# Kernel tuning notes

Hardware: AMD Instinct MI355X
Metric: run time of the kernel (lower is better)

Reference implementation:

```python
import jax, jax.numpy as jnp
import numpy as np

B, H, W, C = 1, 64, 64, 768
HEADS = 12
HD = C // HEADS  # 64


def setup_inputs() -> dict:
    key = jax.random.key(0)
    ks = jax.random.split(key, 11)
    s = 0.02
    return {
        "hidden_states": jax.random.normal(ks[0], (B, H, W, C), jnp.float32),
        "w_q": jax.random.normal(ks[1], (C, C), jnp.float32) * s,
        "b_q": jnp.zeros((C,), jnp.float32),
        "w_k": jax.random.normal(ks[2], (C, C), jnp.float32) * s,
        "b_k": jnp.zeros((C,), jnp.float32),
        "w_v": jax.random.normal(ks[3], (C, C), jnp.float32) * s,
        "b_v": jnp.zeros((C,), jnp.float32),
        "w_o": jax.random.normal(ks[4], (C, C), jnp.float32) * s,
        "b_o": jnp.zeros((C,), jnp.float32),
        "rel_pos_h": jax.random.normal(ks[5], (2 * H - 1, HD), jnp.float32) * s,
        "rel_pos_w": jax.random.normal(ks[6], (2 * W - 1, HD), jnp.float32) * s,
    }


def _get_rel_pos(q_size, k_size, rel_pos):
    # q_size == k_size here, so no interpolation branch; pure gather.
    coords = jnp.arange(q_size)[:, None] - jnp.arange(k_size)[None, :] + (k_size - 1)
    return rel_pos[coords]  # (q_size, k_size, head_dim)


def reference(hidden_states, w_q, b_q, w_k, b_k, w_v, b_v, w_o, b_o, rel_pos_h, rel_pos_w):
    b, h, w, c = hidden_states.shape
    hd = c // HEADS

    def proj(wm, bm):
        y = hidden_states @ wm.T + bm  # (b,h,w,c)
        return y.reshape(b, h * w, HEADS, hd).transpose(0, 2, 1, 3)  # (b,heads,hw,hd)

    q = proj(w_q, b_q)
    k = proj(w_k, b_k)
    v = proj(w_v, b_v)

    # decomposed relative position bias (per head-dim query)
    Rh = _get_rel_pos(h, h, rel_pos_h)  # (h,h,hd)
    Rw = _get_rel_pos(w, w, rel_pos_w)  # (w,w,hd)
    qr = q.reshape(b, HEADS, h, w, hd)
    rel_h = jnp.einsum('bnhwc,hkc->bnhwk', qr, Rh)  # (b,heads,h,w,h)
    rel_w = jnp.einsum('bnhwc,wkc->bnhwk', qr, Rw)  # (b,heads,h,w,w)
    attn_bias = (rel_h[..., :, None] + rel_w[..., None, :]).reshape(b, HEADS, h * w, h * w)

    scale = hd ** -0.5
    scores = jnp.einsum('bnqd,bnkd->bnqk', q, k) * scale + attn_bias
    attn = jax.nn.softmax(scores, axis=-1)
    out = jnp.einsum('bnqk,bnkd->bnqd', attn, v)  # (b,heads,hw,hd)
    out = out.transpose(0, 2, 1, 3).reshape(b, h, w, c)
    return out @ w_o.T + b_o
```

## Files before the change

kernel.cpp:

```cpp
#include <hip/hip_runtime.h>


typedef __attribute__((ext_vector_type(8))) short bf16x8;
typedef __attribute__((ext_vector_type(4))) float f32x4;
typedef __attribute__((ext_vector_type(4))) short s16x4;
typedef __attribute__((ext_vector_type(2))) unsigned int u32x2;

__device__ __forceinline__ float b2f(unsigned short h) {
    union { unsigned int u; float f; } v; v.u = ((unsigned int)h) << 16; return v.f;
}
__device__ __forceinline__ unsigned short f2b(float f) {
    union { float f; unsigned int u; } v; v.f = f;
    unsigned int r = v.u + 0x7FFFu + ((v.u >> 16) & 1u);
    return (unsigned short)(r >> 16);
}
__device__ __forceinline__ void gl_lds16(const void* g, void* l) {
    __builtin_amdgcn_global_load_lds(
        (const __attribute__((address_space(1))) void*)g,
        (__attribute__((address_space(3))) void*)l, 16, 0, 0);
}

__global__ __launch_bounds__(256) void cvt_bf16(
        const float* __restrict__ hs, const float* __restrict__ wq,
        const float* __restrict__ wk, const float* __restrict__ wv,
        const float* __restrict__ wo, const float* __restrict__ rph,
        const float* __restrict__ rpw, unsigned short* __restrict__ dst) {
    const int idx = blockIdx.x * 256 + threadIdx.x;
    if (idx >= 1380320) return;
    const float* src;
    int off;
    if      (idx < 786432)  { src = hs;  off = idx; }
    else if (idx < 933888)  { src = wq;  off = idx - 786432; }
    else if (idx < 1081344) { src = wk;  off = idx - 933888; }
    else if (idx < 1228800) { src = wv;  off = idx - 1081344; }
    else if (idx < 1376256) { src = wo;  off = idx - 1228800; }
    else if (idx < 1378288) { src = rph; off = idx - 1376256; }
    else                    { src = rpw; off = idx - 1378288; }
    const float4 v = ((const float4*)src)[off];
    s16x4 o;
    o[0] = (short)f2b(v.x); o[1] = (short)f2b(v.y);
    o[2] = (short)f2b(v.z); o[3] = (short)f2b(v.w);
    *(s16x4*)(dst + (size_t)idx * 4) = o;
}

__launch_bounds__(256, 3)
__global__ void qkv128(const unsigned short* __restrict__ X,
                       const unsigned short* __restrict__ Wq,
                       const unsigned short* __restrict__ Wk,
                       const unsigned short* __restrict__ Wv,
                       const float* __restrict__ bq,
                       const float* __restrict__ bk,
                       const float* __restrict__ bv,
                       unsigned short* __restrict__ qb,
                       unsigned short* __restrict__ kb,
                       unsigned short* __restrict__ vtb) {
    __shared__ __align__(16) unsigned short sarena[16384];
    const int tid = threadIdx.x, lane = tid & 63, w = tid >> 6;
    const int r = lane & 15, quad = lane >> 4;
    const int nt = blockIdx.x, mt = blockIdx.y, z = blockIdx.z;
    const unsigned short* W  = (z == 0) ? Wq : (z == 1) ? Wk : Wv;
    const float*          Bv = (z == 0) ? bq : (z == 1) ? bk : bv;
    unsigned short*     outp = (z == 0) ? qb : (z == 1) ? kb : vtb;
    const float qsc = (z == 0) ? 0.18033688f : 1.0f;

    const int c0 = w * 64 + lane, c1 = c0 + 256;
    const unsigned short* xs0 = X + (mt * 128 + (c0 & 127)) * 768 + (c0 >> 7) * 8;
    const unsigned short* xs1 = X + (mt * 128 + (c1 & 127)) * 768 + (c1 >> 7) * 8;
    const unsigned short* ws0 = W + (nt * 128 + (c0 & 127)) * 768 + (c0 >> 7) * 8;
    const unsigned short* ws1 = W + (nt * 128 + (c1 & 127)) * 768 + (c1 >> 7) * 8;

    gl_lds16(xs0, &sarena[w * 512]);
    gl_lds16(xs1, &sarena[2048 + w * 512]);
    gl_lds16(ws0, &sarena[4096 + w * 512]);
    gl_lds16(ws1, &sarena[4096 + 2048 + w * 512]);
    __syncthreads();

    const int wr = (w & 1) * 64, wc = (w >> 1) * 64;
    f32x4 acc[4][4] = {};
    int cur = 0;
#pragma unroll 2
    for (int kt = 0; kt < 24; ++kt) {
        if (kt < 23) {
            const int nx = (cur ^ 1) * 8192;
            gl_lds16(xs0 + (kt + 1) * 32, &sarena[nx + w * 512]);
            gl_lds16(xs1 + (kt + 1) * 32, &sarena[nx + 2048 + w * 512]);
            gl_lds16(ws0 + (kt + 1) * 32, &sarena[nx + 4096 + w * 512]);
            gl_lds16(ws1 + (kt + 1) * 32, &sarena[nx + 4096 + 2048 + w * 512]);
        }
        const unsigned short* ab = &sarena[cur * 8192];
        const unsigned short* bb = ab + 4096;
        bf16x8 af[4], bfr[4];
#pragma unroll
        for (int i = 0; i < 4; ++i)
            af[i] = *(const bf16x8*)&ab[(quad * 128 + wr + i * 16 + r) * 8];
#pragma unroll
        for (int j = 0; j < 4; ++j)
            bfr[j] = *(const bf16x8*)&bb[(quad * 128 + wc + j * 16 + r) * 8];
#pragma unroll
        for (int i = 0; i < 4; ++i)
#pragma unroll
            for (int j = 0; j < 4; ++j)
                acc[i][j] = __builtin_amdgcn_mfma_f32_16x16x32_bf16(af[i], bfr[j], acc[i][j], 0, 0, 0);
        __syncthreads();
        cur ^= 1;
    }
    if (z < 2) {
#pragma unroll
        for (int j = 0; j < 4; ++j) {
            const int n = nt * 128 + wc + j * 16 + r;
            const float bias = Bv[n];
            const int nhi = n >> 6, nlo = n & 63;
#pragma unroll
            for (int i = 0; i < 4; ++i) {
#pragma unroll
                for (int reg = 0; reg < 4; ++reg) {
                    const int m = mt * 128 + wr + i * 16 + quad * 4 + reg;
                    outp[(nhi * 4096 + m) * 64 + nlo] = f2b((acc[i][j][reg] + bias) * qsc);
                }
            }
        }
    } else {
#pragma unroll
        for (int pass = 0; pass < 2; ++pass) {
            if ((w >> 1) == pass) {
#pragma unroll
                for (int j = 0; j < 4; ++j) {
                    const int n_l = j * 16 + r;
                    const float bias = Bv[nt * 128 + pass * 64 + n_l];
                    const int sw = (n_l & 7) << 4;
#pragma unroll
                    for (int reg = 0; reg < 4; ++reg) {
                        const int tokb = (wr + (quad * 4 + reg) * 4) ^ sw;
                        u32x2 d2;
                        d2.x = (unsigned int)f2b(acc[0][j][reg] + bias)
                             | ((unsigned int)f2b(acc[1][j][reg] + bias) << 16);
                        d2.y = (unsigned int)f2b(acc[2][j][reg] + bias)
                             | ((unsigned int)f2b(acc[3][j][reg] + bias) << 16);
                        *(u32x2*)&sarena[n_l * 128 + tokb] = d2;
                    }
                }
            }
            __syncthreads();
#pragma unroll
            for (int c = 0; c < 4; ++c) {
                const int u = c * 256 + tid;
                const int n_l = u >> 4, g = u & 15;
                const int phys = n_l * 128 + ((g * 8) ^ ((n_l & 7) << 4));
                bf16x8 val = *(const bf16x8*)&sarena[phys];
                *(bf16x8*)&outp[(size_t)(nt * 128 + pass * 64 + n_l) * 4096
                                + mt * 128 + g * 8] = val;
            }
            __syncthreads();
        }
    }
}

__launch_bounds__(256, 3)
__global__ void out128(const unsigned short* __restrict__ X,
                       const unsigned short* __restrict__ W,
                       const float* __restrict__ Bv,
                       float* __restrict__ out) {
    __shared__ __align__(16) unsigned short sarena[16384];
    const int tid = threadIdx.x, lane = tid & 63, w = tid >> 6;
    const int r = lane & 15, quad = lane >> 4;
    const int nt = blockIdx.x, mt = blockIdx.y;

    const int c0 = w * 64 + lane, c1 = c0 + 256;
    const unsigned short* xs0 = X + (mt * 128 + (c0 & 127)) * 768 + (c0 >> 7) * 8;
    const unsigned short* xs1 = X + (mt * 128 + (c1 & 127)) * 768 + (c1 >> 7) * 8;
    const unsigned short* ws0 = W + (nt * 128 + (c0 & 127)) * 768 + (c0 >> 7) * 8;
    const unsigned short* ws1 = W + (nt * 128 + (c1 & 127)) * 768 + (c1 >> 7) * 8;

    gl_lds16(xs0, &sarena[w * 512]);
    gl_lds16(xs1, &sarena[2048 + w * 512]);
    gl_lds16(ws0, &sarena[4096 + w * 512]);
    gl_lds16(ws1, &sarena[4096 + 2048 + w * 512]);
    __syncthreads();

    const int wr = (w & 1) * 64, wc = (w >> 1) * 64;
    f32x4 acc[4][4] = {};
    int cur = 0;
#pragma unroll 2
    for (int kt = 0; kt < 24; ++kt) {
        if (kt < 23) {
            const int nx = (cur ^ 1) * 8192;
            gl_lds16(xs0 + (kt + 1) * 32, &sarena[nx + w * 512]);
            gl_lds16(xs1 + (kt + 1) * 32, &sarena[nx + 2048 + w * 512]);
            gl_lds16(ws0 + (kt + 1) * 32, &sarena[nx + 4096 + w * 512]);
            gl_lds16(ws1 + (kt + 1) * 32, &sarena[nx + 4096 + 2048 + w * 512]);
        }
        const unsigned short* ab = &sarena[cur * 8192];
        const unsigned short* bb = ab + 4096;
        bf16x8 af[4], bfr[4];
#pragma unroll
        for (int i = 0; i < 4; ++i)
            af[i] = *(const bf16x8*)&ab[(quad * 128 + wr + i * 16 + r) * 8];
#pragma unroll
        for (int j = 0; j < 4; ++j)
            bfr[j] = *(const bf16x8*)&bb[(quad * 128 + wc + j * 16 + r) * 8];
#pragma unroll
        for (int i = 0; i < 4; ++i)
#pragma unroll
            for (int j = 0; j < 4; ++j)
                acc[i][j] = __builtin_amdgcn_mfma_f32_16x16x32_bf16(af[i], bfr[j], acc[i][j], 0, 0, 0);
        __syncthreads();
        cur ^= 1;
    }
#pragma unroll
    for (int j = 0; j < 4; ++j) {
        const int n = nt * 128 + wc + j * 16 + r;
        const float bias = Bv[n];
#pragma unroll
        for (int i = 0; i < 4; ++i) {
#pragma unroll
            for (int reg = 0; reg < 4; ++reg) {
                const int m = mt * 128 + wr + i * 16 + quad * 4 + reg;
                out[m * 768 + n] = acc[i][j][reg] + bias;
            }
        }
    }
}

__launch_bounds__(256, 4)
__global__ void relk(const unsigned short* __restrict__ qbuf,
                     const unsigned short* __restrict__ rph,
                     const unsigned short* __restrict__ rpw,
                     unsigned short* __restrict__ rh,
                     unsigned short* __restrict__ rw) {
    __shared__ __align__(16) unsigned short abuf[8 * 64 * 8];
    __shared__ __align__(16) unsigned short bbuf[8 * 64 * 8];
    const int tid = threadIdx.x;
    const int lane = tid & 63, w = tid >> 6;
    const int r = lane & 15, quad = lane >> 4;
    const int a = blockIdx.x, h = blockIdx.y, mode = blockIdx.z;
    const unsigned short* rp = mode ? rpw : rph;
    const float osc = 8.0f;

#pragma unroll
    for (int gg = 0; gg < 2; ++gg) {
        const int g = w * 2 + gg;
        const int arow = mode ? (h * 4096 + lane * 64 + a) : (h * 4096 + a * 64 + lane);
        gl_lds16(qbuf + arow * 64 + g * 8, &abuf[g * 512]);
        const int bidx = a - lane + 63;
        gl_lds16(rp + bidx * 64 + g * 8, &bbuf[g * 512]);
    }
    __syncthreads();

    f32x4 acc[4] = {};
#pragma unroll
    for (int s = 0; s < 2; ++s) {
        bf16x8 af = *(const bf16x8*)&abuf[((s * 4 + quad) * 64 + w * 16 + r) * 8];
#pragma unroll
        for (int j = 0; j < 4; ++j) {
            bf16x8 bfr = *(const bf16x8*)&bbuf[((s * 4 + quad) * 64 + j * 16 + r) * 8];
            acc[j] = __builtin_amdgcn_mfma_f32_16x16x32_bf16(af, bfr, acc[j], 0, 0, 0);
        }
    }
    unsigned short* out = mode ? rw : rh;
#pragma unroll
    for (int j = 0; j < 4; ++j) {
#pragma unroll
        for (int reg = 0; reg < 4; ++reg) {
            const int m = w * 16 + quad * 4 + reg, n = j * 16 + r;
            const int t = mode ? (h * 4096 + m * 64 + a) : (h * 4096 + a * 64 + m);
            out[t * 64 + n] = f2b(acc[j][reg] * osc);
        }
    }
}

__launch_bounds__(256, 3)
__global__ void attn2(const unsigned short* __restrict__ qbuf,
                      const unsigned short* __restrict__ kbuf,
                      const unsigned short* __restrict__ vtbuf,
                      const unsigned short* __restrict__ rhb,
                      const unsigned short* __restrict__ rwb,
                      float* __restrict__ po, float* __restrict__ lp) {
    __shared__ __align__(16) unsigned short skb[2][4096];
    __shared__ __align__(16) unsigned short svb[2][4096];
    __shared__ __align__(16) unsigned short spb[9216];
    const int tid = threadIdx.x;
    const int lane = tid & 63, w = tid >> 6;
    const int r = lane & 15, quad = lane >> 4;
    const int qt = blockIdx.x, h = blockIdx.y, sp = blockIdx.z;

    {
        const int t0 = sp * 32;
#pragma unroll
        for (int gg = 0; gg < 2; ++gg) {
            const int g = w * 2 + gg;
            gl_lds16(kbuf + (h * 4096 + t0 * 64 + lane) * 64 + g * 8, &skb[0][g * 512]);
            gl_lds16(vtbuf + (h * 64 + lane) * 4096 + t0 * 64 + g * 8, &svb[0][g * 512]);
        }
    }
    const unsigned short* rhp =
        rhb + (size_t)(h * 4096 + qt * 128 + w * 16 + quad * 4) * 64;
    unsigned short rhu[8];
#pragma unroll
    for (int i = 0; i < 8; ++i)
        rhu[i] = rhp[((i >> 2) * 64 + (i & 3)) * 64 + sp * 32];

    bf16x8 qf[2][2];
#pragma unroll
    for (int g = 0; g < 2; ++g) {
        const unsigned short* qrow =
            qbuf + (h * 4096 + qt * 128 + g * 64 + w * 16 + r) * 64;
        qf[g][0] = *(const bf16x8*)(qrow + quad * 8);
        qf[g][1] = *(const bf16x8*)(qrow + 32 + quad * 8);
    }
    float rwL[2][4][4];
#pragma unroll
    for (int g = 0; g < 2; ++g) {
        const unsigned short* rwrow = rwb + (h * 4096 + qt * 128 + g * 64) * 64;
#pragma unroll
        for (int reg = 0; reg < 4; ++reg) {
            const int ql = w * 16 + quad * 4 + reg;
#pragma unroll
            for (int j = 0; j < 4; ++j)
                rwL[g][j][reg] = b2f(rwrow[ql * 64 + j * 16 + r]);
        }
    }
    bf16x8 onesf;
#pragma unroll
    for (int i = 0; i < 8; ++i) onesf[i] = (short)0x3F80;

    f32x4 lacc[2] = {};
    f32x4 oacc[2][4] = {};
    __syncthreads();

    int cur = 0;
#pragma unroll 2
    for (int tl = 0; tl < 32; ++tl) {
        const int t = sp * 32 + tl;
        if (tl < 31) {
#pragma unroll
            for (int gg = 0; gg < 2; ++gg) {
                const int g = w * 2 + gg;
                gl_lds16(kbuf + (h * 4096 + (t + 1) * 64 + lane) * 64 + g * 8,
                         &skb[cur ^ 1][g * 512]);
                gl_lds16(vtbuf + (h * 64 + lane) * 4096 + (t + 1) * 64 + g * 8,
                         &svb[cur ^ 1][g * 512]);
            }
        }
        float rh2f[8];
#pragma unroll
        for (int i = 0; i < 8; ++i) rh2f[i] = b2f(rhu[i]);
        if (tl < 31) {
#pragma unroll
            for (int i = 0; i < 8; ++i)
                rhu[i] = rhp[((i >> 2) * 64 + (i & 3)) * 64 + (t + 1)];
        }
        f32x4 s0[4], s1[4];
#pragma unroll
        for (int j = 0; j < 4; ++j)
#pragma unroll
            for (int reg = 0; reg < 4; ++reg) {
                s0[j][reg] = rh2f[reg]     + rwL[0][j][reg];
                s1[j][reg] = rh2f[4 + reg] + rwL[1][j][reg];
            }
        __builtin_amdgcn_s_setprio(1);
#pragma unroll
        for (int s2 = 0; s2 < 2; ++s2) {
#pragma unroll
            for (int j = 0; j < 4; ++j) {
                bf16x8 kf = *(const bf16x8*)&skb[cur][((s2 * 4 + quad) * 64 + j * 16 + r) * 8];
                s0[j] = __builtin_amdgcn_mfma_f32_16x16x32_bf16(qf[0][s2], kf, s0[j], 0, 0, 0);
                s1[j] = __builtin_amdgcn_mfma_f32_16x16x32_bf16(qf[1][s2], kf, s1[j], 0, 0, 0);
            }
        }
        __builtin_amdgcn_s_setprio(0);
#pragma unroll
        for (int g = 0; g < 2; ++g) {
#pragma unroll
            for (int reg = 0; reg < 4; ++reg) {
                unsigned int u[4];
#pragma unroll
                for (int j = 0; j < 4; ++j) {
                    const float p = __builtin_amdgcn_exp2f(g ? s1[j][reg] : s0[j][reg]);
                    union { float f; unsigned int q; } cv; cv.f = p;
                    u[j] = cv.q;
                }
                u32x2 d;
                d.x = __builtin_amdgcn_perm(u[1], u[0], 0x07060302);
                d.y = __builtin_amdgcn_perm(u[3], u[2], 0x07060302);
                *(u32x2*)&spb[g * 4608 + w * 1152 + (quad * 4 + reg) * 72 + r * 4] = d;
            }
        }
        __builtin_amdgcn_s_setprio(1);
#pragma unroll
        for (int s = 0; s < 2; ++s) {
            bf16x8 pf0 = *(const bf16x8*)&spb[w * 1152 + r * 72 + s * 32 + quad * 8];
            bf16x8 pf1 = *(const bf16x8*)&spb[4608 + w * 1152 + r * 72 + s * 32 + quad * 8];
            lacc[0] = __builtin_amdgcn_mfma_f32_16x16x32_bf16(pf0, onesf, lacc[0], 0, 0, 0);
            lacc[1] = __builtin_amdgcn_mfma_f32_16x16x32_bf16(pf1, onesf, lacc[1], 0, 0, 0);
#pragma unroll
            for (int j = 0; j < 4; ++j) {
                bf16x8 vf = *(const bf16x8*)&svb[cur][((s * 4 + quad) * 64 + j * 16 + r) * 8];
                oacc[0][j] = __builtin_amdgcn_mfma_f32_16x16x32_bf16(pf0, vf, oacc[0][j], 0, 0, 0);
                oacc[1][j] = __builtin_amdgcn_mfma_f32_16x16x32_bf16(pf1, vf, oacc[1][j], 0, 0, 0);
            }
        }
        __builtin_amdgcn_s_setprio(0);

        __syncthreads();
        cur ^= 1;
    }
    const size_t pbase = ((size_t)(sp * 12 + h) * 4096 + qt * 128);
#pragma unroll
    for (int g = 0; g < 2; ++g) {
        const int qrow = g * 64 + w * 16 + quad * 4;
#pragma unroll
        for (int reg = 0; reg < 4; ++reg) {
#pragma unroll
            for (int j = 0; j < 4; ++j)
                po[(pbase + qrow + reg) * 64 + j * 16 + r] = oacc[g][j][reg];
            if (r == 0) lp[pbase + qrow + reg] = lacc[g][reg];
        }
    }
}

__global__ __launch_bounds__(256) void combine(const float* __restrict__ po,
                                               const float* __restrict__ lp,
                                               unsigned short* __restrict__ ab) {
    const unsigned int idx = blockIdx.x * 256 + threadIdx.x;
    const unsigned int tok = idx / 96u;
    const unsigned int part = idx - tok * 96u;
    const int c = part * 8, h = c >> 6, d = c & 63;
    const float* p0 = po + ((size_t)h * 4096 + tok) * 64 + d;
    const float* p1 = po + ((size_t)(12 + h) * 4096 + tok) * 64 + d;
    const float inv = 1.f / (lp[h * 4096 + tok] + lp[(12 + h) * 4096 + tok]);
    const float4 a0 = *(const float4*)p0, b0 = *(const float4*)(p0 + 4);
    const float4 a1 = *(const float4*)p1, b1 = *(const float4*)(p1 + 4);
    s16x4 o0, o1;
    o0[0] = (short)f2b((a0.x + a1.x) * inv); o0[1] = (short)f2b((a0.y + a1.y) * inv);
    o0[2] = (short)f2b((a0.z + a1.z) * inv); o0[3] = (short)f2b((a0.w + a1.w) * inv);
    o1[0] = (short)f2b((b0.x + b1.x) * inv); o1[1] = (short)f2b((b0.y + b1.y) * inv);
    o1[2] = (short)f2b((b0.z + b1.z) * inv); o1[3] = (short)f2b((b0.w + b1.w) * inv);
    unsigned short* dst = ab + (size_t)tok * 768 + c;
    *(s16x4*)dst = o0;
    *(s16x4*)(dst + 4) = o1;
}

extern "C" void kernel_launch(void* const* d_in, const int* in_sizes, int n_in,
                              void* d_out, int out_size, void* d_ws, size_t ws_size,
                              hipStream_t stream) {
    const float* hs  = (const float*)d_in[0];
    const float* wq  = (const float*)d_in[1];
    const float* bq  = (const float*)d_in[2];
    const float* wk  = (const float*)d_in[3];
    const float* bk  = (const float*)d_in[4];
    const float* wv  = (const float*)d_in[5];
    const float* bv  = (const float*)d_in[6];
    const float* wo  = (const float*)d_in[7];
    const float* bo  = (const float*)d_in[8];
    const float* rph = (const float*)d_in[9];
    const float* rpw = (const float*)d_in[10];

    unsigned short* ws = (unsigned short*)d_ws;
    const int HS = 3145728, WN = 589824, RP = 8128;
    const int HB = 12 * 4096 * 64;
    unsigned short* hsb  = ws;
    unsigned short* wqb  = hsb  + HS;
    unsigned short* wkb  = wqb  + WN;
    unsigned short* wvb  = wkb  + WN;
    unsigned short* wob  = wvb  + WN;
    unsigned short* rphb = wob  + WN;
    unsigned short* rpwb = rphb + RP;
    unsigned short* qb   = rpwb + RP;
    unsigned short* kb   = qb   + HB;
    unsigned short* vtb  = kb   + HB;
    unsigned short* rhb  = vtb  + HB;
    unsigned short* rwb  = rhb  + HB;
    unsigned short* ab   = rwb  + HB;
    float* po = (float*)(ab + HB);
    float* lp = po + 2 * 12 * 4096 * 64;

    cvt_bf16<<<dim3((1380320 + 255) / 256), 256, 0, stream>>>(
        hs, wq, wk, wv, wo, rph, rpw, hsb);
    qkv128<<<dim3(6, 32, 3), 256, 0, stream>>>(
        hsb, wqb, wkb, wvb, bq, bk, bv, qb, kb, vtb);
    relk<<<dim3(64, 12, 2), 256, 0, stream>>>(qb, rphb, rpwb, rhb, rwb);
    attn2<<<dim3(32, 12, 2), 256, 0, stream>>>(qb, kb, vtb, rhb, rwb, po, lp);
    combine<<<dim3(1536), 256, 0, stream>>>(po, lp, ab);
    out128<<<dim3(6, 32), 256, 0, stream>>>(ab, wob, bo, (float*)d_out);
}
```

Measured before the change: 241.0 us.

## Prefetch K/V tiles through registers into single LDS buffer

Replaces the double-buffered direct global-to-LDS async loads of K and V tiles with register prefetch: the next tile is loaded into registers during compute, then written to a single LDS buffer after a barrier. This halves LDS use for K/V, which could allow more resident blocks, and uses wider 16-byte-per-lane loads. In exchange it adds a second __syncthreads per iteration, extra VGPR pressure, and explicit LDS store instructions, and it drops the unroll-by-2.

```diff
diff --git a/kernel.cpp b/kernel.cpp
--- a/kernel.cpp
+++ b/kernel.cpp
@@ -5,6 +5,7 @@
 typedef __attribute__((ext_vector_type(4))) float f32x4;
 typedef __attribute__((ext_vector_type(4))) short s16x4;
 typedef __attribute__((ext_vector_type(2))) unsigned int u32x2;
+typedef __attribute__((ext_vector_type(4))) unsigned int u32x4;
 
 __device__ __forceinline__ float b2f(unsigned short h) {
     union { unsigned int u; float f; } v; v.u = ((unsigned int)h) << 16; return v.f;
@@ -275,22 +276,23 @@
                       const unsigned short* __restrict__ rhb,
                       const unsigned short* __restrict__ rwb,
                       float* __restrict__ po, float* __restrict__ lp) {
-    __shared__ __align__(16) unsigned short skb[2][4096];
-    __shared__ __align__(16) unsigned short svb[2][4096];
+    __shared__ __align__(16) unsigned short skb[4096];
+    __shared__ __align__(16) unsigned short svb[4096];
     __shared__ __align__(16) unsigned short spb[9216];
     const int tid = threadIdx.x;
     const int lane = tid & 63, w = tid >> 6;
     const int r = lane & 15, quad = lane >> 4;
     const int qt = blockIdx.x, h = blockIdx.y, sp = blockIdx.z;
 
+    const unsigned short* ksrc = kbuf + (size_t)(h * 4096 + lane) * 64 + w * 16;
+    const unsigned short* vsrc = vtbuf + (size_t)(h * 64 + lane) * 4096 + w * 16;
+    u32x4 kp0, kp1, vp0, vp1;
     {
         const int t0 = sp * 32;
-#pragma unroll
-        for (int gg = 0; gg < 2; ++gg) {
-            const int g = w * 2 + gg;
-            gl_lds16(kbuf + (h * 4096 + t0 * 64 + lane) * 64 + g * 8, &skb[0][g * 512]);
-            gl_lds16(vtbuf + (h * 64 + lane) * 4096 + t0 * 64 + g * 8, &svb[0][g * 512]);
-        }
+        kp0 = *(const u32x4*)(ksrc + (size_t)t0 * 4096);
+        kp1 = *(const u32x4*)(ksrc + (size_t)t0 * 4096 + 8);
+        vp0 = *(const u32x4*)(vsrc + t0 * 64);
+        vp1 = *(const u32x4*)(vsrc + t0 * 64 + 8);
     }
     const unsigned short* rhp =
         rhb + (size_t)(h * 4096 + qt * 128 + w * 16 + quad * 4) * 64;
@@ -325,21 +327,19 @@
 
     f32x4 lacc[2] = {};
     f32x4 oacc[2][4] = {};
+    *(u32x4*)&skb[(w * 128 + lane) * 8]      = kp0;
+    *(u32x4*)&skb[(w * 128 + 64 + lane) * 8] = kp1;
+    *(u32x4*)&svb[(w * 128 + lane) * 8]      = vp0;
+    *(u32x4*)&svb[(w * 128 + 64 + lane) * 8] = vp1;
     __syncthreads();
 
-    int cur = 0;
-#pragma unroll 2
     for (int tl = 0; tl < 32; ++tl) {
         const int t = sp * 32 + tl;
         if (tl < 31) {
-#pragma unroll
-            for (int gg = 0; gg < 2; ++gg) {
-                const int g = w * 2 + gg;
-                gl_lds16(kbuf + (h * 4096 + (t + 1) * 64 + lane) * 64 + g * 8,
-                         &skb[cur ^ 1][g * 512]);
-                gl_lds16(vtbuf + (h * 64 + lane) * 4096 + (t + 1) * 64 + g * 8,
-                         &svb[cur ^ 1][g * 512]);
-            }
+            kp0 = *(const u32x4*)(ksrc + (size_t)(t + 1) * 4096);
+            kp1 = *(const u32x4*)(ksrc + (size_t)(t + 1) * 4096 + 8);
+            vp0 = *(const u32x4*)(vsrc + (t + 1) * 64);
+            vp1 = *(const u32x4*)(vsrc + (t + 1) * 64 + 8);
         }
         float rh2f[8];
 #pragma unroll
@@ -362,7 +362,7 @@
         for (int s2 = 0; s2 < 2; ++s2) {
 #pragma unroll
             for (int j = 0; j < 4; ++j) {
-                bf16x8 kf = *(const bf16x8*)&skb[cur][((s2 * 4 + quad) * 64 + j * 16 + r) * 8];
+                bf16x8 kf = *(const bf16x8*)&skb[((s2 * 4 + quad) * 64 + j * 16 + r) * 8];
                 s0[j] = __builtin_amdgcn_mfma_f32_16x16x32_bf16(qf[0][s2], kf, s0[j], 0, 0, 0);
                 s1[j] = __builtin_amdgcn_mfma_f32_16x16x32_bf16(qf[1][s2], kf, s1[j], 0, 0, 0);
             }
@@ -394,7 +394,7 @@
             lacc[1] = __builtin_amdgcn_mfma_f32_16x16x32_bf16(pf1, onesf, lacc[1], 0, 0, 0);
 #pragma unroll
             for (int j = 0; j < 4; ++j) {
-                bf16x8 vf = *(const bf16x8*)&svb[cur][((s * 4 + quad) * 64 + j * 16 + r) * 8];
+                bf16x8 vf = *(const bf16x8*)&svb[((s * 4 + quad) * 64 + j * 16 + r) * 8];
                 oacc[0][j] = __builtin_amdgcn_mfma_f32_16x16x32_bf16(pf0, vf, oacc[0][j], 0, 0, 0);
                 oacc[1][j] = __builtin_amdgcn_mfma_f32_16x16x32_bf16(pf1, vf, oacc[1][j], 0, 0, 0);
             }
@@ -402,7 +402,13 @@
         __builtin_amdgcn_s_setprio(0);
 
         __syncthreads();
-        cur ^= 1;
+        if (tl < 31) {
+            *(u32x4*)&skb[(w * 128 + lane) * 8]      = kp0;
+            *(u32x4*)&skb[(w * 128 + 64 + lane) * 8] = kp1;
+            *(u32x4*)&svb[(w * 128 + lane) * 8]      = vp0;
+            *(u32x4*)&svb[(w * 128 + 64 + lane) * 8] = vp1;
+        }
+        __syncthreads();
     }
     const size_t pbase = ((size_t)(sp * 12 + h) * 4096 + qt * 128);
 #pragma unroll
```

After: 242.1 us. About the same (+0.5%).

## Load K/V fragments directly to registers and swizzle attention block order

Applied to the files above, without the earlier changes.

The attention kernel stops staging K and V tiles through double-buffered LDS with per-iteration barriers. Each lane now loads its MFMA K/V fragments straight from global memory into registers, prefetching the next K tile during compute. The rel-h bias slice is preloaded into LDS once instead of being fetched per iteration. The grid is flattened and remapped so blocks sharing the same head/K-range are spread across XCDs for L2 locality. The cost is more global/L2 traffic per block, since K/V are no longer shared across waves, plus extra register pressure.

```diff
diff --git a/kernel.cpp b/kernel.cpp
--- a/kernel.cpp
+++ b/kernel.cpp
@@ -275,30 +275,21 @@
                       const unsigned short* __restrict__ rhb,
                       const unsigned short* __restrict__ rwb,
                       float* __restrict__ po, float* __restrict__ lp) {
-    __shared__ __align__(16) unsigned short skb[2][4096];
-    __shared__ __align__(16) unsigned short svb[2][4096];
     __shared__ __align__(16) unsigned short spb[9216];
+    __shared__ __align__(16) unsigned short srh[4096];
     const int tid = threadIdx.x;
     const int lane = tid & 63, w = tid >> 6;
     const int r = lane & 15, quad = lane >> 4;
-    const int qt = blockIdx.x, h = blockIdx.y, sp = blockIdx.z;
-
-    {
-        const int t0 = sp * 32;
-#pragma unroll
-        for (int gg = 0; gg < 2; ++gg) {
-            const int g = w * 2 + gg;
-            gl_lds16(kbuf + (h * 4096 + t0 * 64 + lane) * 64 + g * 8, &skb[0][g * 512]);
-            gl_lds16(vtbuf + (h * 64 + lane) * 4096 + t0 * 64 + g * 8, &svb[0][g * 512]);
-        }
-    }
-    const unsigned short* rhp =
-        rhb + (size_t)(h * 4096 + qt * 128 + w * 16 + quad * 4) * 64;
-    unsigned short rhu[8];
-#pragma unroll
-    for (int i = 0; i < 8; ++i)
-        rhu[i] = rhp[((i >> 2) * 64 + (i & 3)) * 64 + sp * 32];
-
+    const int bid = blockIdx.x;
+    const int g768 = (bid & 7) * 96 + (bid >> 3);
+    const int h = g768 >> 6, sp = (g768 >> 5) & 1, qt = g768 & 31;
+
+#pragma unroll
+    for (int i = 0; i < 2; ++i) {
+        const int ql = (w & 1) * 64 + lane;
+        gl_lds16(rhb + (h * 4096 + qt * 128 + ql) * 64 + (sp * 4 + i * 2 + (w >> 1)) * 8,
+                 &srh[(i * 256 + w * 64) * 8]);
+    }
     bf16x8 qf[2][2];
 #pragma unroll
     for (int g = 0; g < 2; ++g) {
@@ -323,32 +314,29 @@
 #pragma unroll
     for (int i = 0; i < 8; ++i) onesf[i] = (short)0x3F80;
 
+    const unsigned short* klane = kbuf + ((size_t)h * 4096 + r) * 64 + quad * 8;
+    const unsigned short* vlane = vtbuf + ((size_t)h * 64 + r) * 4096 + quad * 8;
+
     f32x4 lacc[2] = {};
     f32x4 oacc[2][4] = {};
     __syncthreads();
 
-    int cur = 0;
-#pragma unroll 2
+    bf16x8 kf[8], vf[8];
+    {
+        const int t0 = sp * 32;
+#pragma unroll
+        for (int i = 0; i < 8; ++i)
+            kf[i] = *(const bf16x8*)(klane + (size_t)t0 * 4096
+                                     + (i & 3) * 1024 + (i >> 2) * 32);
+    }
+
     for (int tl = 0; tl < 32; ++tl) {
         const int t = sp * 32 + tl;
-        if (tl < 31) {
-#pragma unroll
-            for (int gg = 0; gg < 2; ++gg) {
-                const int g = w * 2 + gg;
-                gl_lds16(kbuf + (h * 4096 + (t + 1) * 64 + lane) * 64 + g * 8,
-                         &skb[cur ^ 1][g * 512]);
-                gl_lds16(vtbuf + (h * 64 + lane) * 4096 + (t + 1) * 64 + g * 8,
-                         &svb[cur ^ 1][g * 512]);
-            }
-        }
         float rh2f[8];
 #pragma unroll
-        for (int i = 0; i < 8; ++i) rh2f[i] = b2f(rhu[i]);
-        if (tl < 31) {
-#pragma unroll
-            for (int i = 0; i < 8; ++i)
-                rhu[i] = rhp[((i >> 2) * 64 + (i & 3)) * 64 + (t + 1)];
-        }
+        for (int i = 0; i < 8; ++i)
+            rh2f[i] = b2f(srh[((tl >> 3) * 128 + (i >> 2) * 64 + w * 16
+                               + quad * 4 + (i & 3)) * 8 + (t & 7)]);
         f32x4 s0[4], s1[4];
 #pragma unroll
         for (int j = 0; j < 4; ++j)
@@ -362,12 +350,21 @@
         for (int s2 = 0; s2 < 2; ++s2) {
 #pragma unroll
             for (int j = 0; j < 4; ++j) {
-                bf16x8 kf = *(const bf16x8*)&skb[cur][((s2 * 4 + quad) * 64 + j * 16 + r) * 8];
-                s0[j] = __builtin_amdgcn_mfma_f32_16x16x32_bf16(qf[0][s2], kf, s0[j], 0, 0, 0);
-                s1[j] = __builtin_amdgcn_mfma_f32_16x16x32_bf16(qf[1][s2], kf, s1[j], 0, 0, 0);
+                s0[j] = __builtin_amdgcn_mfma_f32_16x16x32_bf16(qf[0][s2], kf[s2 * 4 + j], s0[j], 0, 0, 0);
+                s1[j] = __builtin_amdgcn_mfma_f32_16x16x32_bf16(qf[1][s2], kf[s2 * 4 + j], s1[j], 0, 0, 0);
             }
         }
         __builtin_amdgcn_s_setprio(0);
+#pragma unroll
+        for (int i = 0; i < 8; ++i)
+            vf[i] = *(const bf16x8*)(vlane + (size_t)(i & 3) * 65536
+                                     + t * 64 + (i >> 2) * 32);
+        if (tl < 31) {
+#pragma unroll
+            for (int i = 0; i < 8; ++i)
+                kf[i] = *(const bf16x8*)(klane + (size_t)(t + 1) * 4096
+                                         + (i & 3) * 1024 + (i >> 2) * 32);
+        }
 #pragma unroll
         for (int g = 0; g < 2; ++g) {
 #pragma unroll
@@ -394,15 +391,11 @@
             lacc[1] = __builtin_amdgcn_mfma_f32_16x16x32_bf16(pf1, onesf, lacc[1], 0, 0, 0);
 #pragma unroll
             for (int j = 0; j < 4; ++j) {
-                bf16x8 vf = *(const bf16x8*)&svb[cur][((s * 4 + quad) * 64 + j * 16 + r) * 8];
-                oacc[0][j] = __builtin_amdgcn_mfma_f32_16x16x32_bf16(pf0, vf, oacc[0][j], 0, 0, 0);
-                oacc[1][j] = __builtin_amdgcn_mfma_f32_16x16x32_bf16(pf1, vf, oacc[1][j], 0, 0, 0);
+                oacc[0][j] = __builtin_amdgcn_mfma_f32_16x16x32_bf16(pf0, vf[s * 4 + j], oacc[0][j], 0, 0, 0);
+                oacc[1][j] = __builtin_amdgcn_mfma_f32_16x16x32_bf16(pf1, vf[s * 4 + j], oacc[1][j], 0, 0, 0);
             }
         }
         __builtin_amdgcn_s_setprio(0);
-
-        __syncthreads();
-        cur ^= 1;
     }
     const size_t pbase = ((size_t)(sp * 12 + h) * 4096 + qt * 128);
 #pragma unroll
@@ -479,7 +472,7 @@
     qkv128<<<dim3(6, 32, 3), 256, 0, stream>>>(
         hsb, wqb, wkb, wvb, bq, bk, bv, qb, kb, vtb);
     relk<<<dim3(64, 12, 2), 256, 0, stream>>>(qb, rphb, rpwb, rhb, rwb);
-    attn2<<<dim3(32, 12, 2), 256, 0, stream>>>(qb, kb, vtb, rhb, rwb, po, lp);
+    attn2<<<dim3(768), 256, 0, stream>>>(qb, kb, vtb, rhb, rwb, po, lp);
     combine<<<dim3(1536), 256, 0, stream>>>(po, lp, ab);
     out128<<<dim3(6, 32), 256, 0, stream>>>(ab, wob, bo, (float*)d_out);
 }
```

Result: slower. 431.6 us (+79.1%).
